# Kernel optimization log

Measured on AMD Instinct MI355X. Metric: run time of the kernel, lower is better.

## Reference

```python
import jax, jax.numpy as jnp
import numpy as np

E = 1024        # embedding_dim
H = 16          # num_heads
DR = 1          # downsample_rate
INT = E // DR   # internal_dim
HD = INT // H   # head dim
B, NQ, NK = 4, 2048, 2048


def setup_inputs() -> dict:
    key = jax.random.key(0)
    ks = jax.random.split(key, 11)
    s_in = 1.0 / np.sqrt(E)
    s_int = 1.0 / np.sqrt(INT)
    return {
        "q": jax.random.normal(ks[0], (B, NQ, E), jnp.float32),
        "k": jax.random.normal(ks[1], (B, NK, E), jnp.float32),
        "v": jax.random.normal(ks[2], (B, NK, E), jnp.float32),
        "wq": jax.random.normal(ks[3], (E, INT), jnp.float32) * s_in,
        "bq": jnp.zeros((INT,), jnp.float32),
        "wk": jax.random.normal(ks[4], (E, INT), jnp.float32) * s_in,
        "bk": jnp.zeros((INT,), jnp.float32),
        "wv": jax.random.normal(ks[5], (E, INT), jnp.float32) * s_in,
        "bv": jnp.zeros((INT,), jnp.float32),
        "wo": jax.random.normal(ks[6], (INT, E), jnp.float32) * s_int,
        "bo": jnp.zeros((E,), jnp.float32),
    }


def _heads(x):
    # (B, N, INT) -> (B, H, N, HD)
    b, n, c = x.shape
    return x.reshape(b, n, H, c // H).transpose(0, 2, 1, 3)


def reference(q, k, v, wq, bq, wk, bk, wv, bv, wo, bo):
    qh = _heads(q @ wq + bq)          # (B,H,NQ,HD)
    kh = _heads(k @ wk + bk)          # (B,H,NK,HD)
    vh = _heads(v @ wv + bv)          # (B,H,NK,HD)
    scale = 1.0 / np.sqrt(HD)
    attn = jnp.einsum('bhqd,bhkd->bhqk', qh, kh) * scale  # (B,H,NQ,NK)
    attn = jax.nn.softmax(attn, axis=-1)
    out = jnp.einsum('bhqk,bhkd->bhqd', attn, vh)          # (B,H,NQ,HD)
    out = out.transpose(0, 2, 1, 3).reshape(q.shape[0], qh.shape[2], INT)
    return out @ wo + bo
```

## Files before the change

kernel.cpp:

```cpp
#include <hip/hip_runtime.h>
#include <hip/hip_bf16.h>
#include <cstdint>
#include <cstddef>

typedef __bf16 bf16_t;
typedef __bf16 bf16x8 __attribute__((ext_vector_type(8)));
typedef float f32x4 __attribute__((ext_vector_type(4)));
typedef float f32x16 __attribute__((ext_vector_type(16)));
typedef uint32_t u32;

#define EDIM 1024
#define HH 16
#define HD 64
#define NSEQ 2048
#define QSCALE 0.18033688011f

__device__ __forceinline__ void async_copy16(const bf16_t* gsrc, bf16_t* lds_dst) {
    __builtin_amdgcn_global_load_lds(
        (const __attribute__((address_space(1))) uint32_t*)gsrc,
        (__attribute__((address_space(3))) uint32_t*)lds_dst,
        16, 0, 0);
}

__device__ __forceinline__ bf16x8 cvt8(float4 x, float4 y) {
    bf16x8 v = {(bf16_t)x.x, (bf16_t)x.y, (bf16_t)x.z, (bf16_t)x.w,
                (bf16_t)y.x, (bf16_t)y.y, (bf16_t)y.z, (bf16_t)y.w};
    return v;
}

__global__ void transpose_all(const float* __restrict__ w0, const float* __restrict__ w1,
                              const float* __restrict__ w2, const float* __restrict__ w3,
                              bf16_t* __restrict__ o0, bf16_t* __restrict__ o1,
                              bf16_t* __restrict__ o2, bf16_t* __restrict__ o3) {
    __shared__ bf16_t t[64][65];
    const float* in;
    bf16_t* out;
    switch (blockIdx.z) {
        case 0: in = w0; out = o0; break;
        case 1: in = w1; out = o1; break;
        case 2: in = w2; out = o2; break;
        default: in = w3; out = o3; break;
    }
    const int tid = threadIdx.x;
    const int kt = blockIdx.x, nt = blockIdx.y;
    #pragma unroll
    for (int i = 0; i < 16; i++) {
        int idx = i * 256 + tid;
        int r = idx >> 6, c = idx & 63;
        t[r][c] = (bf16_t)in[(size_t)(kt * 64 + r) * 1024 + nt * 64 + c];
    }
    __syncthreads();
    #pragma unroll
    for (int i = 0; i < 16; i++) {
        int idx = i * 256 + tid;
        int r = idx >> 6, c = idx & 63;
        out[(size_t)(nt * 64 + r) * 1024 + kt * 64 + c] = t[c][r];
    }
}

__global__ __launch_bounds__(256, 2)
void gemm_qkv(const float* __restrict__ Aq, const float* __restrict__ Ak,
              const float* __restrict__ Av,
              const bf16_t* __restrict__ Wq, const bf16_t* __restrict__ Wk,
              const bf16_t* __restrict__ Wv,
              const float* __restrict__ bq, const float* __restrict__ bk,
              const float* __restrict__ bv,
              bf16_t* __restrict__ Qh, bf16_t* __restrict__ Kh,
              bf16_t* __restrict__ Vt) {
    constexpr int BM = 128, BN = 128, BK = 64, K = 1024, NT = K / BK;
    __shared__ bf16_t Asm[2][BM * BK];
    __shared__ bf16_t Bsm[2][BN * BK];
    const int tid = threadIdx.x;
    const int wave = tid >> 6, lane = tid & 63;
    const int quad = lane >> 4, l15 = lane & 15;
    const int bx = blockIdx.x, by = blockIdx.y;
    const int mt = (by >> 3) * 8 + bx;
    const int n0 = (by & 7) * BN;
    const int wt = mt >> 6;
    const int m0 = (mt - wt * 64) * BM;
    const int wm = (wave & 1) * 64, wn = (wave >> 1) * 64;

    const float*  A    = wt == 0 ? Aq : (wt == 1 ? Ak : Av);
    const bf16_t* Bt   = wt == 0 ? Wq : (wt == 1 ? Wk : Wv);
    const float*  bias = wt == 0 ? bq : (wt == 1 ? bk : bv);
    bf16_t*       Cout = wt == 0 ? Qh : (wt == 1 ? Kh : Vt);
    const float oscale = wt == 0 ? QSCALE : 1.0f;

    f32x4 acc[4][4] = {};
    float4 ar[8];

    auto loadA = [&](int t) {
        const int k0 = t * BK;
        #pragma unroll
        for (int i = 0; i < 4; i++) {
            int s = i * 256 + tid;
            int row = s >> 3, kc = (s & 7) ^ (row & 7);
            const float* sp = A + (size_t)(m0 + row) * K + k0 + kc * 8;
            ar[2 * i]     = *(const float4*)sp;
            ar[2 * i + 1] = *(const float4*)(sp + 4);
        }
    };
    auto writeA = [&](int buf) {
        #pragma unroll
        for (int i = 0; i < 4; i++) {
            int s = i * 256 + tid;
            *(bf16x8*)&Asm[buf][s * 8] = cvt8(ar[2 * i], ar[2 * i + 1]);
        }
    };
    auto stageB = [&](int t, int buf) {
        const int k0 = t * BK;
        #pragma unroll
        for (int i = 0; i < 4; i++) {
            int s = i * 256 + tid;
            int row = s >> 3, kc = (s & 7) ^ (row & 7);
            async_copy16(Bt + (size_t)(n0 + row) * K + k0 + kc * 8, &Bsm[buf][s * 8]);
        }
    };

    loadA(0);
    stageB(0, 0);
    writeA(0);
    stageB(1, 1);
    asm volatile("s_waitcnt vmcnt(4)" ::: "memory");
    loadA(1);
    asm volatile("s_waitcnt lgkmcnt(0)" ::: "memory");
    __builtin_amdgcn_s_barrier();
    __builtin_amdgcn_sched_barrier(0);

    for (int t = 0; t < NT; ++t) {
        const int buf = t & 1;
        bf16x8 af[2][4], bfr[2][4];
        #pragma unroll
        for (int ks = 0; ks < 2; ks++) {
            #pragma unroll
            for (int mi = 0; mi < 4; mi++) {
                int row = wm + mi * 16 + l15;
                int g = ks * 4 + quad;
                af[ks][mi] = *(const bf16x8*)&Asm[buf][row * BK + ((g ^ (row & 7)) * 8)];
            }
            #pragma unroll
            for (int ni = 0; ni < 4; ni++) {
                int row = wn + ni * 16 + l15;
                int g = ks * 4 + quad;
                bfr[ks][ni] = *(const bf16x8*)&Bsm[buf][row * BK + ((g ^ (row & 7)) * 8)];
            }
        }
        #pragma unroll
        for (int ks = 0; ks < 2; ks++)
            #pragma unroll
            for (int mi = 0; mi < 4; mi++)
                #pragma unroll
                for (int ni = 0; ni < 4; ni++)
                    acc[mi][ni] = __builtin_amdgcn_mfma_f32_16x16x32_bf16(
                        af[ks][mi], bfr[ks][ni], acc[mi][ni], 0, 0, 0);

        if (t + 1 < NT) {
            __builtin_amdgcn_s_barrier();
            __builtin_amdgcn_sched_barrier(0);
            writeA(buf ^ 1);
            if (t + 2 < NT) {
                stageB(t + 2, buf);
                asm volatile("s_waitcnt vmcnt(4)" ::: "memory");
                loadA(t + 2);
            } else {
                asm volatile("s_waitcnt vmcnt(0)" ::: "memory");
            }
            asm volatile("s_waitcnt lgkmcnt(0)" ::: "memory");
            __builtin_amdgcn_s_barrier();
            __builtin_amdgcn_sched_barrier(0);
        }
    }

    #pragma unroll
    for (int mi = 0; mi < 4; mi++) {
        #pragma unroll
        for (int ni = 0; ni < 4; ni++) {
            #pragma unroll
            for (int r = 0; r < 4; r++) {
                int m = m0 + wm + mi * 16 + quad * 4 + r;
                int nch = n0 + wn + ni * 16 + l15;
                float v = (acc[mi][ni][r] + bias[nch]) * oscale;
                int b = m >> 11, n = m & 2047;
                int h = nch >> 6, d = nch & 63;
                if (wt < 2)
                    Cout[(((size_t)(b * HH + h)) * NSEQ + n) * HD + d] = (bf16_t)v;
                else
                    Cout[(((size_t)(b * HH + h)) * HD + d) * NSEQ + n] = (bf16_t)v;
            }
        }
    }
}

__global__ __launch_bounds__(256, 2)
void gemm_out(const bf16_t* __restrict__ A, const bf16_t* __restrict__ Bt,
              const float* __restrict__ bias, float* __restrict__ C) {
    constexpr int BM = 128, BN = 128, BK = 64, K = 1024, N = 1024, NT = K / BK;
    __shared__ bf16_t Asm[2][BM * BK];
    __shared__ bf16_t Bsm[2][BN * BK];
    const int tid = threadIdx.x;
    const int wave = tid >> 6, lane = tid & 63;
    const int quad = lane >> 4, l15 = lane & 15;
    const int bx = blockIdx.x, by = blockIdx.y;
    const int n0 = (by & 7) * BN;
    const int m0 = ((by >> 3) * 8 + bx) * BM;
    const int wm = (wave & 1) * 64, wn = (wave >> 1) * 64;

    f32x4 acc[4][4] = {};

    auto stage = [&](int t, int buf) {
        const int k0 = t * BK;
        #pragma unroll
        for (int i = 0; i < 4; i++) {
            int s = i * 256 + tid;
            int row = s >> 3, kc = (s & 7) ^ (row & 7);
            async_copy16(A + (size_t)(m0 + row) * K + k0 + kc * 8, &Asm[buf][s * 8]);
        }
        #pragma unroll
        for (int i = 0; i < 4; i++) {
            int s = i * 256 + tid;
            int row = s >> 3, kc = (s & 7) ^ (row & 7);
            async_copy16(Bt + (size_t)(n0 + row) * K + k0 + kc * 8, &Bsm[buf][s * 8]);
        }
    };

    stage(0, 0);
    stage(1, 1);
    asm volatile("s_waitcnt vmcnt(8)" ::: "memory");
    __builtin_amdgcn_s_barrier();
    __builtin_amdgcn_sched_barrier(0);

    for (int t = 0; t < NT; ++t) {
        const int buf = t & 1;
        bf16x8 af[2][4], bfr[2][4];
        #pragma unroll
        for (int ks = 0; ks < 2; ks++) {
            #pragma unroll
            for (int mi = 0; mi < 4; mi++) {
                int row = wm + mi * 16 + l15;
                int g = ks * 4 + quad;
                af[ks][mi] = *(const bf16x8*)&Asm[buf][row * BK + ((g ^ (row & 7)) * 8)];
            }
            #pragma unroll
            for (int ni = 0; ni < 4; ni++) {
                int row = wn + ni * 16 + l15;
                int g = ks * 4 + quad;
                bfr[ks][ni] = *(const bf16x8*)&Bsm[buf][row * BK + ((g ^ (row & 7)) * 8)];
            }
        }
        #pragma unroll
        for (int ks = 0; ks < 2; ks++)
            #pragma unroll
            for (int mi = 0; mi < 4; mi++)
                #pragma unroll
                for (int ni = 0; ni < 4; ni++)
                    acc[mi][ni] = __builtin_amdgcn_mfma_f32_16x16x32_bf16(
                        af[ks][mi], bfr[ks][ni], acc[mi][ni], 0, 0, 0);

        if (t + 1 < NT) {
            __builtin_amdgcn_s_barrier();
            __builtin_amdgcn_sched_barrier(0);
            if (t + 2 < NT) {
                stage(t + 2, buf);
                asm volatile("s_waitcnt vmcnt(8)" ::: "memory");
            } else {
                asm volatile("s_waitcnt vmcnt(0)" ::: "memory");
            }
            asm volatile("s_waitcnt lgkmcnt(0)" ::: "memory");
            __builtin_amdgcn_s_barrier();
            __builtin_amdgcn_sched_barrier(0);
        }
    }

    #pragma unroll
    for (int mi = 0; mi < 4; mi++) {
        #pragma unroll
        for (int ni = 0; ni < 4; ni++) {
            #pragma unroll
            for (int r = 0; r < 4; r++) {
                int m = m0 + wm + mi * 16 + quad * 4 + r;
                int nch = n0 + wn + ni * 16 + l15;
                C[(size_t)m * N + nch] = acc[mi][ni][r] + bias[nch];
            }
        }
    }
}

union PW { u32 w[4]; bf16x8 v; };

__device__ __forceinline__ u32 pack_bf16(float lo, float hi) {
    union { bf16_t h[2]; u32 u; } x;
    x.h[0] = (bf16_t)lo;
    x.h[1] = (bf16_t)hi;
    return x.u;
}

__device__ __forceinline__ void half_swap(u32& a, u32& b) {
    auto r = __builtin_amdgcn_permlane32_swap(a, b, false, false);
    a = r[0];
    b = r[1];
}

__device__ __forceinline__ void softmax_pack(const f32x16 sa, float* lp,
                                             PW& f0, PW& f1) {
    float p[16];
    #pragma unroll
    for (int r = 0; r < 16; r++) {
        p[r] = __builtin_amdgcn_exp2f(sa[r]);
        lp[r & 3] += p[r];
    }
    u32 x0 = pack_bf16(p[0],  p[1]),  x1 = pack_bf16(p[2],  p[3]);
    u32 x2 = pack_bf16(p[4],  p[5]),  x3 = pack_bf16(p[6],  p[7]);
    u32 x4 = pack_bf16(p[8],  p[9]),  x5 = pack_bf16(p[10], p[11]);
    u32 x6 = pack_bf16(p[12], p[13]), x7 = pack_bf16(p[14], p[15]);
    half_swap(x0, x2); half_swap(x1, x3);
    half_swap(x4, x6); half_swap(x5, x7);
    f0.w[0] = x0; f0.w[1] = x1; f0.w[2] = x2; f0.w[3] = x3;
    f1.w[0] = x4; f1.w[1] = x5; f1.w[2] = x6; f1.w[3] = x7;
}

__global__ __launch_bounds__(256, 4)
void attn_kernel(const bf16_t* __restrict__ Qh, const bf16_t* __restrict__ Kh,
                 const bf16_t* __restrict__ Vt, bf16_t* __restrict__ out) {
    __shared__ bf16_t Ks[2][64 * 64];
    __shared__ bf16_t Vs[2][64 * 64];
    const int tid = threadIdx.x, wave = tid >> 6, lane = tid & 63;
    const int l31 = lane & 31, hi = lane >> 5;
    const int B = blockIdx.x;
    const int qt = (B >> 3) & 15;
    const int bh = (B >> 7) * 8 + (B & 7);
    const int b = bh >> 4, h = bh & 15;

    const bf16_t* kbase = Kh + (size_t)bh * NSEQ * HD;
    const bf16_t* vbase = Vt + (size_t)bh * HD * NSEQ;

    bf16x8 qf[4];
    {
        const bf16_t* qrow =
            Qh + ((size_t)bh * NSEQ + qt * 128 + wave * 32 + l31) * HD + hi * 8;
        #pragma unroll
        for (int s = 0; s < 4; s++) qf[s] = *(const bf16x8*)(qrow + s * 16);
    }

    const bf16_t *ks0, *ks1, *vs0, *vs1;
    {
        int r0 = tid >> 3, c0 = tid & 7;
        int s1 = tid + 256;
        int r1 = s1 >> 3, c1 = s1 & 7;
        ks0 = kbase + r0 * HD + (c0 ^ (r0 & 7)) * 8;
        ks1 = kbase + r1 * HD + (c1 ^ (r1 & 7)) * 8;
        vs0 = vbase + (size_t)r0 * NSEQ + (c0 ^ (r0 & 7)) * 8;
        vs1 = vbase + (size_t)r1 * NSEQ + (c1 ^ (r1 & 7)) * 8;
    }

    async_copy16(ks0, &Ks[0][tid * 8]);
    async_copy16(ks1, &Ks[0][(tid + 256) * 8]);
    async_copy16(vs0, &Vs[0][tid * 8]);
    async_copy16(vs1, &Vs[0][(tid + 256) * 8]);

    f32x16 oacc[2] = {};
    float lp[4] = {};

    for (int t = 0; t < 32; t++) {
        const int cur = t & 1;
        __syncthreads();

        if (t < 31) {
            ks0 += 64 * HD; ks1 += 64 * HD;
            vs0 += 64;      vs1 += 64;
            async_copy16(ks0, &Ks[cur ^ 1][tid * 8]);
            async_copy16(ks1, &Ks[cur ^ 1][(tid + 256) * 8]);
            async_copy16(vs0, &Vs[cur ^ 1][tid * 8]);
            async_copy16(vs1, &Vs[cur ^ 1][(tid + 256) * 8]);
        }

        const f32x16 zero = {};
        f32x16 sacc0, sacc1;
        {
            int g = hi;
            int row0 = l31, row1 = 32 + l31;
            bf16x8 ak0 = *(const bf16x8*)&Ks[cur][row0 * 64 + ((g ^ (row0 & 7)) * 8)];
            bf16x8 ak1 = *(const bf16x8*)&Ks[cur][row1 * 64 + ((g ^ (row1 & 7)) * 8)];
            __builtin_amdgcn_s_setprio(1);
            sacc0 = __builtin_amdgcn_mfma_f32_32x32x16_bf16(ak0, qf[0], zero, 0, 0, 0);
            sacc1 = __builtin_amdgcn_mfma_f32_32x32x16_bf16(ak1, qf[0], zero, 0, 0, 0);
            __builtin_amdgcn_s_setprio(0);
        }
        #pragma unroll
        for (int s = 1; s < 4; s++) {
            int g = s * 2 + hi;
            int row0 = l31;
            int row1 = 32 + l31;
            bf16x8 ak0 = *(const bf16x8*)&Ks[cur][row0 * 64 + ((g ^ (row0 & 7)) * 8)];
            bf16x8 ak1 = *(const bf16x8*)&Ks[cur][row1 * 64 + ((g ^ (row1 & 7)) * 8)];
            __builtin_amdgcn_s_setprio(1);
            sacc0 = __builtin_amdgcn_mfma_f32_32x32x16_bf16(ak0, qf[s], sacc0, 0, 0, 0);
            sacc1 = __builtin_amdgcn_mfma_f32_32x32x16_bf16(ak1, qf[s], sacc1, 0, 0, 0);
            __builtin_amdgcn_s_setprio(0);
        }

        PW pa[4];
        softmax_pack(sacc0, lp, pa[0], pa[1]);
        softmax_pack(sacc1, lp, pa[2], pa[3]);

        #pragma unroll
        for (int dt = 0; dt < 2; dt++) {
            #pragma unroll
            for (int ks = 0; ks < 4; ks++) {
                int row = dt * 32 + l31;
                int g = ks * 2 + hi;
                bf16x8 bv = *(const bf16x8*)&Vs[cur][row * 64 + ((g ^ (row & 7)) * 8)];
                __builtin_amdgcn_s_setprio(1);
                oacc[dt] = __builtin_amdgcn_mfma_f32_32x32x16_bf16(
                    pa[ks].v, bv, oacc[dt], 0, 0, 0);
                __builtin_amdgcn_s_setprio(0);
            }
        }
    }

    float lsum = (lp[0] + lp[1]) + (lp[2] + lp[3]);
    lsum += __shfl_xor(lsum, 32, 64);
    float linv = 1.f / lsum;
    float rinv[16];
    #pragma unroll
    for (int r = 0; r < 16; r++) {
        int q = (r & 3) + 8 * (r >> 2) + 4 * hi;
        rinv[r] = __shfl(linv, q, 64);
    }

    const int n0 = qt * 128 + wave * 32;
    #pragma unroll
    for (int dt = 0; dt < 2; dt++) {
        int c = h * 64 + dt * 32 + l31;
        #pragma unroll
        for (int r = 0; r < 16; r++) {
            int q = (r & 3) + 8 * (r >> 2) + 4 * hi;
            out[((size_t)b * NSEQ + n0 + q) * EDIM + c] = (bf16_t)(oacc[dt][r] * rinv[r]);
        }
    }
}

extern "C" void kernel_launch(void* const* d_in, const int* in_sizes, int n_in,
                              void* d_out, int out_size, void* d_ws, size_t ws_size,
                              hipStream_t stream) {
    const float* q  = (const float*)d_in[0];
    const float* k  = (const float*)d_in[1];
    const float* v  = (const float*)d_in[2];
    const float* wq = (const float*)d_in[3];
    const float* bq = (const float*)d_in[4];
    const float* wk = (const float*)d_in[5];
    const float* bk = (const float*)d_in[6];
    const float* wv = (const float*)d_in[7];
    const float* bv = (const float*)d_in[8];
    const float* wo = (const float*)d_in[9];
    const float* bo = (const float*)d_in[10];
    float* out = (float*)d_out;

    char* ws = (char*)d_ws;
    bf16_t* wqt = (bf16_t*)(ws + ((size_t)0  << 20));
    bf16_t* wkt = (bf16_t*)(ws + ((size_t)2  << 20));
    bf16_t* wvt = (bf16_t*)(ws + ((size_t)4  << 20));
    bf16_t* wot = (bf16_t*)(ws + ((size_t)6  << 20));

    bf16_t* Qh  = (bf16_t*)(ws + ((size_t)8  << 20));
    bf16_t* Kh  = (bf16_t*)(ws + ((size_t)24 << 20));
    bf16_t* Vt  = (bf16_t*)(ws + ((size_t)40 << 20));
    bf16_t* ao  = (bf16_t*)(ws + ((size_t)56 << 20));

    transpose_all<<<dim3(16, 16, 4), dim3(256), 0, stream>>>(wq, wk, wv, wo,
                                                             wqt, wkt, wvt, wot);

    gemm_qkv<<<dim3(8, 192), dim3(256), 0, stream>>>(q, k, v, wqt, wkt, wvt,
                                                     bq, bk, bv, Qh, Kh, Vt);

    attn_kernel<<<1024, dim3(256), 0, stream>>>(Qh, Kh, Vt, ao);

    gemm_out<<<dim3(8, 64), dim3(256), 0, stream>>>(ao, wot, bo, out);
}
```

Measured before the change: 345.9 us.

## Pre-convert QKV inputs to bf16 and use async LDS-loading projection GEMM

Adds a separate kernel that converts the fp32 q/k/v activations to bf16 in workspace. The projection GEMM can then stream its A and B tiles straight into LDS with global_load_lds async copies and double buffering, instead of converting on the fly in registers. It costs an extra pass over the activations (read fp32, write bf16) and more workspace. The new path runs only when the workspace holds at least 120 MiB, otherwise the old kernel is used.

After: 334.4 us. -3.3%, faster.

```diff
diff --git a/kernel.cpp b/kernel.cpp
--- a/kernel.cpp
+++ b/kernel.cpp
@@ -26,6 +26,23 @@
     bf16x8 v = {(bf16_t)x.x, (bf16_t)x.y, (bf16_t)x.z, (bf16_t)x.w,
                 (bf16_t)y.x, (bf16_t)y.y, (bf16_t)y.z, (bf16_t)y.w};
     return v;
+}
+
+__global__ void cvt3_f32_bf16(const float* __restrict__ q, const float* __restrict__ k,
+                              const float* __restrict__ v,
+                              bf16_t* __restrict__ xq, bf16_t* __restrict__ xk,
+                              bf16_t* __restrict__ xv) {
+    const float* in;
+    bf16_t* out;
+    switch (blockIdx.y) {
+        case 0: in = q; out = xq; break;
+        case 1: in = k; out = xk; break;
+        default: in = v; out = xv; break;
+    }
+    size_t i = ((size_t)blockIdx.x * 256 + threadIdx.x) * 8;
+    float4 x = *(const float4*)(in + i);
+    float4 y = *(const float4*)(in + i + 4);
+    *(bf16x8*)(out + i) = cvt8(x, y);
 }
 
 __global__ void transpose_all(const float* __restrict__ w0, const float* __restrict__ w1,
@@ -55,6 +72,120 @@
         int idx = i * 256 + tid;
         int r = idx >> 6, c = idx & 63;
         out[(size_t)(nt * 64 + r) * 1024 + kt * 64 + c] = t[c][r];
+    }
+}
+
+__global__ __launch_bounds__(256, 2)
+void gemm_qkv_async(const bf16_t* __restrict__ Xq, const bf16_t* __restrict__ Xk,
+                    const bf16_t* __restrict__ Xv,
+                    const bf16_t* __restrict__ Wq, const bf16_t* __restrict__ Wk,
+                    const bf16_t* __restrict__ Wv,
+                    const float* __restrict__ bq, const float* __restrict__ bk,
+                    const float* __restrict__ bv,
+                    bf16_t* __restrict__ Qh, bf16_t* __restrict__ Kh,
+                    bf16_t* __restrict__ Vt) {
+    constexpr int BM = 128, BN = 128, BK = 64, K = 1024, NT = K / BK;
+    __shared__ bf16_t Asm[2][BM * BK];
+    __shared__ bf16_t Bsm[2][BN * BK];
+    const int tid = threadIdx.x;
+    const int wave = tid >> 6, lane = tid & 63;
+    const int quad = lane >> 4, l15 = lane & 15;
+    const int bx = blockIdx.x, by = blockIdx.y;
+    const int mt = (by >> 3) * 8 + bx;
+    const int n0 = (by & 7) * BN;
+    const int wt = mt >> 6;
+    const int m0 = (mt - wt * 64) * BM;
+    const int wm = (wave & 1) * 64, wn = (wave >> 1) * 64;
+
+    const bf16_t* A    = wt == 0 ? Xq : (wt == 1 ? Xk : Xv);
+    const bf16_t* Bt   = wt == 0 ? Wq : (wt == 1 ? Wk : Wv);
+    const float*  bias = wt == 0 ? bq : (wt == 1 ? bk : bv);
+    bf16_t*       Cout = wt == 0 ? Qh : (wt == 1 ? Kh : Vt);
+    const float oscale = wt == 0 ? QSCALE : 1.0f;
+
+    f32x4 acc[4][4] = {};
+
+    auto stage = [&](int t, int buf) {
+        const int k0 = t * BK;
+        #pragma unroll
+        for (int i = 0; i < 4; i++) {
+            int s = i * 256 + tid;
+            int row = s >> 3, kc = (s & 7) ^ (row & 7);
+            async_copy16(A + (size_t)(m0 + row) * K + k0 + kc * 8, &Asm[buf][s * 8]);
+        }
+        #pragma unroll
+        for (int i = 0; i < 4; i++) {
+            int s = i * 256 + tid;
+            int row = s >> 3, kc = (s & 7) ^ (row & 7);
+            async_copy16(Bt + (size_t)(n0 + row) * K + k0 + kc * 8, &Bsm[buf][s * 8]);
+        }
+    };
+
+    stage(0, 0);
+    stage(1, 1);
+    asm volatile("s_waitcnt vmcnt(8)" ::: "memory");
+    __builtin_amdgcn_s_barrier();
+    __builtin_amdgcn_sched_barrier(0);
+
+    for (int t = 0; t < NT; ++t) {
+        const int buf = t & 1;
+        bf16x8 af[2][4], bfr[2][4];
+        #pragma unroll
+        for (int ks = 0; ks < 2; ks++) {
+            #pragma unroll
+            for (int mi = 0; mi < 4; mi++) {
+                int row = wm + mi * 16 + l15;
+                int g = ks * 4 + quad;
+                af[ks][mi] = *(const bf16x8*)&Asm[buf][row * BK + ((g ^ (row & 7)) * 8)];
+            }
+            #pragma unroll
+            for (int ni = 0; ni < 4; ni++) {
+                int row = wn + ni * 16 + l15;
+                int g = ks * 4 + quad;
+                bfr[ks][ni] = *(const bf16x8*)&Bsm[buf][row * BK + ((g ^ (row & 7)) * 8)];
+            }
+        }
+        #pragma unroll
+        for (int ks = 0; ks < 2; ks++)
+            #pragma unroll
+            for (int mi = 0; mi < 4; mi++)
+                #pragma unroll
+                for (int ni = 0; ni < 4; ni++)
+                    acc[mi][ni] = __builtin_amdgcn_mfma_f32_16x16x32_bf16(
+                        af[ks][mi], bfr[ks][ni], acc[mi][ni], 0, 0, 0);
+
+        if (t + 1 < NT) {
+            __builtin_amdgcn_s_barrier();
+            __builtin_amdgcn_sched_barrier(0);
+            if (t + 2 < NT) {
+                stage(t + 2, buf);
+                asm volatile("s_waitcnt vmcnt(8)" ::: "memory");
+            } else {
+                asm volatile("s_waitcnt vmcnt(0)" ::: "memory");
+            }
+            asm volatile("s_waitcnt lgkmcnt(0)" ::: "memory");
+            __builtin_amdgcn_s_barrier();
+            __builtin_amdgcn_sched_barrier(0);
+        }
+    }
+
+    #pragma unroll
+    for (int mi = 0; mi < 4; mi++) {
+        #pragma unroll
+        for (int ni = 0; ni < 4; ni++) {
+            #pragma unroll
+            for (int r = 0; r < 4; r++) {
+                int m = m0 + wm + mi * 16 + quad * 4 + r;
+                int nch = n0 + wn + ni * 16 + l15;
+                float v = (acc[mi][ni][r] + bias[nch]) * oscale;
+                int b = m >> 11, n = m & 2047;
+                int h = nch >> 6, d = nch & 63;
+                if (wt < 2)
+                    Cout[(((size_t)(b * HH + h)) * NSEQ + n) * HD + d] = (bf16_t)v;
+                else
+                    Cout[(((size_t)(b * HH + h)) * HD + d) * NSEQ + n] = (bf16_t)v;
+            }
+        }
     }
 }
 
@@ -465,12 +596,24 @@
     bf16_t* Kh  = (bf16_t*)(ws + ((size_t)24 << 20));
     bf16_t* Vt  = (bf16_t*)(ws + ((size_t)40 << 20));
     bf16_t* ao  = (bf16_t*)(ws + ((size_t)56 << 20));
+    bf16_t* Xq  = (bf16_t*)(ws + ((size_t)72 << 20));
+    bf16_t* Xk  = (bf16_t*)(ws + ((size_t)88 << 20));
+    bf16_t* Xv  = (bf16_t*)(ws + ((size_t)104 << 20));
+
+    const bool big = ws_size >= ((size_t)120 << 20);
 
     transpose_all<<<dim3(16, 16, 4), dim3(256), 0, stream>>>(wq, wk, wv, wo,
                                                              wqt, wkt, wvt, wot);
 
-    gemm_qkv<<<dim3(8, 192), dim3(256), 0, stream>>>(q, k, v, wqt, wkt, wvt,
-                                                     bq, bk, bv, Qh, Kh, Vt);
+    if (big) {
+        cvt3_f32_bf16<<<dim3(4096, 3), dim3(256), 0, stream>>>(q, k, v, Xq, Xk, Xv);
+        gemm_qkv_async<<<dim3(8, 192), dim3(256), 0, stream>>>(Xq, Xk, Xv,
+                                                               wqt, wkt, wvt,
+                                                               bq, bk, bv, Qh, Kh, Vt);
+    } else {
+        gemm_qkv<<<dim3(8, 192), dim3(256), 0, stream>>>(q, k, v, wqt, wkt, wvt,
+                                                         bq, bk, bv, Qh, Kh, Vt);
+    }
 
     attn_kernel<<<1024, dim3(256), 0, stream>>>(Qh, Kh, Vt, ao);
 
```
